# Kernel tuning notes

Measured on AMD Instinct MI355X. Metric: run time of the kernel, lower is better.

The kernel has to match this reference:

```python
import jax, jax.numpy as jnp
import numpy as np

EPS = 1e-6
NUM_SPECIAL = 4
NUM_HEADS = 16


def _rms_norm(x, w, eps=EPS):
    # x: [..., d], normalize over last dim
    var = jnp.mean(jnp.square(x), axis=-1, keepdims=True)
    return x * jax.lax.rsqrt(var + eps) * w


def _rotate_half(x):
    d = x.shape[-1] // 2
    return jnp.concatenate([-x[..., d:], x[..., :d]], axis=-1)


def _apply_rotary(q, k, cos, sin):
    # q,k: [B,H,N,hd]; cos,sin: [N,hd] -> broadcast [1,1,N,hd]
    cos = cos[None, None, :, :]
    sin = sin[None, None, :, :]
    q_out = q * cos + _rotate_half(q) * sin
    k_out = k * cos + _rotate_half(k) * sin
    return q_out, k_out


def _make_2d_mask(seq_len, num_special, window):
    # special tokens attend / are attended fully; patches use 2D local box
    patch_len = seq_len - num_special
    gs = int(round(patch_len ** 0.5))
    idx = jnp.arange(seq_len)
    special = idx < num_special
    p = idx - num_special
    row = p // gs
    col = p % gs
    special_case = special[:, None] | special[None, :]
    swa = (jnp.abs(row[:, None] - row[None, :]) <= window) & (
        jnp.abs(col[:, None] - col[None, :]) <= window)
    return special_case | swa  # [N, N] bool


def setup_inputs() -> dict:
    key = jax.random.key(0)
    ks = jax.random.split(key, 7)
    B, N, C = 4, 1028, 1024
    hd = C // NUM_HEADS
    return {
        "hidden_states": jax.random.normal(ks[0], (B, N, C), dtype=jnp.float32),
        "cos": jax.random.uniform(ks[1], (N, hd), dtype=jnp.float32),
        "sin": jax.random.uniform(ks[2], (N, hd), dtype=jnp.float32),
        "qkv_w": jax.random.normal(ks[3], (3 * C, C), dtype=jnp.float32) * (C ** -0.5),
        "out_w": jax.random.normal(ks[4], (C, C), dtype=jnp.float32) * (C ** -0.5),
        "norm_q_w": jnp.ones((hd,), dtype=jnp.float32),
        "norm_k_w": jnp.ones((hd,), dtype=jnp.float32),
        "sliding_window": 2,
    }


def reference(hidden_states, cos, sin, qkv_w, out_w, norm_q_w, norm_k_w, sliding_window):
    B, N, C = hidden_states.shape
    H = NUM_HEADS
    hd = C // H

    # fused QKV projection (nn.Linear: x @ W^T)
    qkv = jnp.einsum('bnc,dc->bnd', hidden_states, qkv_w)
    qkv = qkv.reshape(B, N, 3, H, hd).transpose(2, 0, 3, 1, 4)  # [3,B,H,N,hd]
    q, k, v = qkv[0], qkv[1], qkv[2]

    # per-head-dim RMSNorm on q and k
    q = _rms_norm(q, norm_q_w)
    k = _rms_norm(k, norm_k_w)

    # RoPE
    q, k = _apply_rotary(q, k, cos, sin)

    # 2D sliding-window + special-token mask
    mask = _make_2d_mask(N, NUM_SPECIAL, sliding_window)  # [N,N]

    scale = 1.0 / jnp.sqrt(jnp.asarray(hd, dtype=q.dtype))
    scores = jnp.einsum('bhqd,bhkd->bhqk', q, k) * scale
    neg = jnp.asarray(jnp.finfo(scores.dtype).min, dtype=scores.dtype)
    scores = jnp.where(mask[None, None, :, :], scores, neg)
    probs = jax.nn.softmax(scores, axis=-1)
    attn = jnp.einsum('bhqk,bhkd->bhqd', probs, v)  # [B,H,N,hd]

    attn = attn.transpose(0, 2, 1, 3).reshape(B, N, C)
    return jnp.einsum('bnc,dc->bnd', attn, out_w)
```

## Files before the change

kernel.cpp:

```cpp
#include <hip/hip_runtime.h>
#include <hip/hip_bf16.h>
#include <stdint.h>

typedef __bf16 bf16;
typedef __attribute__((ext_vector_type(8))) __bf16 bf16x8;
typedef __attribute__((ext_vector_type(4))) __bf16 bf16x4;
typedef __attribute__((ext_vector_type(4))) float f32x4;

#define NSEQ 1028
#define CDIM 1024
#define NHEADS 16
#define HD 64
#define BHN 64
#define NPAD 1088
#define M_REAL 4112
#define MTILES 33

static __device__ __forceinline__ void async_copy16(bf16* lds, const bf16* g) {
  __builtin_amdgcn_global_load_lds(
      (const __attribute__((address_space(1))) uint32_t*)g,
      (__attribute__((address_space(3))) uint32_t*)lds, 16, 0, 0);
}

__global__ __launch_bounds__(256) void cast3_kernel(
    const float* __restrict__ s0, bf16* __restrict__ d0, long n0,
    const float* __restrict__ s1, bf16* __restrict__ d1, long n1,
    const float* __restrict__ s2, bf16* __restrict__ d2, long n2) {
  long total = n0 + n1 + n2;
  long t = (long)blockIdx.x * 256 + threadIdx.x;
  long stride = (long)gridDim.x * 256;
  for (long j = t * 4; j < total; j += stride * 4) {
    const float* s; bf16* d; long jj = j;
    if (jj < n0) { s = s0; d = d0; }
    else if (jj < n0 + n1) { s = s1; d = d1; jj -= n0; }
    else { s = s2; d = d2; jj -= n0 + n1; }
    float4 v = *(const float4*)(s + jj);
    bf16x4 o;
    o[0] = (bf16)v.x; o[1] = (bf16)v.y; o[2] = (bf16)v.z; o[3] = (bf16)v.w;
    *(bf16x4*)(d + jj) = o;
  }
}

template <int EPI, int NSTRIP, int BN, int DEPTH>
__global__ __launch_bounds__(256, 4) void gemm_bf16_kernel(
    const bf16* __restrict__ A, const bf16* __restrict__ Bm,
    bf16* __restrict__ q_bf, bf16* __restrict__ k_bf, bf16* __restrict__ v_raw,
    float* __restrict__ outF,
    const float* __restrict__ cosb, const float* __restrict__ sinb,
    const float* __restrict__ nqw, const float* __restrict__ nkw) {
  constexpr int K = CDIM;
  constexpr int N = NSTRIP * 8 * BN;
  constexpr int HN = BN / 2;
  constexpr int NJ = HN / 16;
  constexpr int BSLOTS = (BN * 4) / 256;
  constexpr int LPS = 2 + BSLOTS;
  constexpr int NBUF = DEPTH + 1;
  __shared__ __attribute__((aligned(16))) bf16 As[NBUF][128 * 32];
  __shared__ __attribute__((aligned(16))) bf16 Bs[NBUF][BN * 32];
  const int tid = threadIdx.x;
  const int lane = tid & 63;
  const int wid = tid >> 6;
  const int wr = wid >> 1, wc = wid & 1;
  const int l15 = lane & 15, l4 = lane >> 4;

  const int xcd = blockIdx.x & 7;
  const int pos = blockIdx.x >> 3;
  const int nloc = pos % NSTRIP;
  const int mi = pos / NSTRIP;
  const int n0 = (xcd * NSTRIP + nloc) * BN;
  const int m0 = (mi < MTILES - 1) ? (mi << 7) : (M_REAL - 128);

  f32x4 acc[4][NJ] = {};

  size_t a_base[2], b_base[BSLOTS];
#pragma unroll
  for (int s = 0; s < 2; s++) {
    int c = tid + s * 256;
    int u = c ^ ((c >> 3) & 7);
    a_base[s] = (size_t)(m0 + (u >> 2)) * K + ((u & 3) << 3);
  }
#pragma unroll
  for (int s = 0; s < BSLOTS; s++) {
    int c = tid + s * 256;
    int u = c ^ ((c >> 3) & 7);
    b_base[s] = (size_t)(n0 + (u >> 2)) * K + ((u & 3) << 3);
  }

#define STAGE(bufi, ktof)                                                   \
  {                                                                         \
    _Pragma("unroll")                                                       \
    for (int s = 0; s < 2; s++)                                             \
      async_copy16(&As[bufi][(tid + s * 256) * 8], A + a_base[s] + (ktof)); \
    _Pragma("unroll")                                                       \
    for (int s = 0; s < BSLOTS; s++)                                        \
      async_copy16(&Bs[bufi][(tid + s * 256) * 8], Bm + b_base[s] + (ktof));\
  }

  const int nt = K >> 5;
#pragma unroll
  for (int d = 0; d < DEPTH; d++) STAGE(d, d << 5);

  for (int t = 0; t < nt; ++t) {
    if (t + DEPTH < nt) STAGE((t + DEPTH) % NBUF, (t + DEPTH) << 5);
    const int left = nt - 1 - t;
    if (left >= DEPTH) {
      asm volatile("s_waitcnt vmcnt(%0)" :: "i"(DEPTH * LPS) : "memory");
    } else if (left == 1) {
      asm volatile("s_waitcnt vmcnt(%0)" :: "i"(LPS) : "memory");
    } else {
      asm volatile("s_waitcnt vmcnt(0)" ::: "memory");
    }
    __builtin_amdgcn_s_barrier();

    const int cur = t % NBUF;
    bf16x8 af[4], bfr[NJ];
#pragma unroll
    for (int i = 0; i < 4; i++) {
      int u = ((wr * 64 + i * 16 + l15) << 2) | l4;
      af[i] = *(const bf16x8*)&As[cur][(u ^ ((u >> 3) & 7)) << 3];
    }
#pragma unroll
    for (int j = 0; j < NJ; j++) {
      int u = ((wc * HN + j * 16 + l15) << 2) | l4;
      bfr[j] = *(const bf16x8*)&Bs[cur][(u ^ ((u >> 3) & 7)) << 3];
    }

#pragma unroll
    for (int i = 0; i < 4; i++)
#pragma unroll
      for (int j = 0; j < NJ; j++)
        acc[i][j] = __builtin_amdgcn_mfma_f32_16x16x32_bf16(af[i], bfr[j], acc[i][j], 0, 0, 0);

    asm volatile("s_waitcnt lgkmcnt(0)" ::: "memory");
    __builtin_amdgcn_s_barrier();
  }
#undef STAGE

  if (EPI == 0) {
    const int d_base = n0 + wc * 64;
    const int tsel = d_base >> 10;
    const int hh = (d_base & 1023) >> 6;
    if (tsel == 2) {
#pragma unroll
      for (int i = 0; i < 4; i++)
#pragma unroll
        for (int r = 0; r < 4; r++) {
          int m = m0 + wr * 64 + i * 16 + l4 * 4 + r;
          int b = m / NSEQ, n = m % NSEQ;
          size_t rb = ((size_t)(b * NHEADS + hh) * NSEQ + n) * HD;
#pragma unroll
          for (int j = 0; j < NJ; j++)
            v_raw[rb + j * 16 + l15] = (bf16)acc[i][j][r];
        }
    } else {
      const float* wn = (tsel == 0) ? nqw : nkw;
      bf16* dst = (tsel == 0) ? q_bf : k_bf;
      float wv[NJ];
#pragma unroll
      for (int j = 0; j < NJ; j++) wv[j] = wn[j * 16 + l15];
#pragma unroll
      for (int i = 0; i < 4; i++)
#pragma unroll
        for (int r = 0; r < 4; r++) {
          int m = m0 + wr * 64 + i * 16 + l4 * 4 + r;
          float ss = 0.0f;
#pragma unroll
          for (int j = 0; j < NJ; j++) { float x = acc[i][j][r]; ss += x * x; }
          ss += __shfl_xor(ss, 1);
          ss += __shfl_xor(ss, 2);
          ss += __shfl_xor(ss, 4);
          ss += __shfl_xor(ss, 8);
          float rms = rsqrtf(ss * (1.0f / HD) + 1e-6f);
          int b = m / NSEQ, n = m % NSEQ;
          float qn[NJ];
#pragma unroll
          for (int j = 0; j < NJ; j++) qn[j] = acc[i][j][r] * rms * wv[j];
          size_t rb = ((size_t)(b * NHEADS + hh) * NPAD + n) * HD;
#pragma unroll
          for (int j = 0; j < NJ; j++) {
            float c = cosb[n * HD + j * 16 + l15];
            float s = sinb[n * HD + j * 16 + l15];
            float rot = (j < 2) ? -qn[j + 2] : qn[j - 2];
            dst[rb + j * 16 + l15] = (bf16)(qn[j] * c + rot * s);
          }
        }
    }
  } else {
#pragma unroll
    for (int i = 0; i < 4; i++)
#pragma unroll
      for (int j = 0; j < NJ; j++) {
        int d = n0 + wc * HN + j * 16 + l15;
        int mrow = m0 + wr * 64 + i * 16 + l4 * 4;
#pragma unroll
        for (int r = 0; r < 4; r++) {
          int m = mrow + r;
          outF[(size_t)m * N + d] = acc[i][j][r];
        }
      }
  }
}

__global__ __launch_bounds__(256) void v_transpose_kernel(const bf16* __restrict__ v_raw,
                                                          bf16* __restrict__ vT) {
  __shared__ bf16 tile[64][65];
  int bh = blockIdx.y, c = blockIdx.x;
  int tid = threadIdx.x;
#pragma unroll
  for (int jj = 0; jj < 16; jj++) {
    int idx = tid + jj * 256;
    int i = idx >> 6, e = idx & 63;
    int n = (c == 0) ? i : (64 * c - 60 + i);
    bool ok = (c == 0) ? (i < 4) : (n < NSEQ);
    tile[i][e] = ok ? v_raw[((size_t)bh * NSEQ + n) * HD + e] : (bf16)0.0f;
  }
  __syncthreads();
#pragma unroll
  for (int jj = 0; jj < 16; jj++) {
    int idx = tid + jj * 256;
    int e = idx >> 6, i = idx & 63;
    vT[((size_t)bh * HD + e) * NPAD + 64 * c + i] = tile[i][e];
  }
}

__global__ __launch_bounds__(256) void attn_kernel(
    const bf16* __restrict__ Q, const bf16* __restrict__ Kb, const bf16* __restrict__ Vt,
    bf16* __restrict__ att, const int* __restrict__ winp) {
  __shared__ __attribute__((aligned(16))) bf16 P_s[4][16][72];
  __shared__ __attribute__((aligned(16))) bf16 KV[2][2][64 * 64];
  const int bh = blockIdx.y, qt = blockIdx.x;
  const int W = winp[0];
  const int tid = threadIdx.x, w = tid >> 6, lane = tid & 63;
  const int l15 = lane & 15, l4 = lane >> 4;
  const size_t qkbase = (size_t)bh * NPAD * HD;
  const size_t vtb = (size_t)bh * HD * NPAD;
  const bool is_spec = (qt == 16);
  const int b = bh >> 4, h = bh & 15;

  const int qrow0 = is_spec ? 0 : (4 + qt * 64 + w * 16);
  bf16x8 aq0 = *(const bf16x8*)&Q[qkbase + (size_t)(qrow0 + l15) * HD + l4 * 8];
  bf16x8 aq1 = *(const bf16x8*)&Q[qkbase + (size_t)(qrow0 + l15) * HD + 32 + l4 * 8];

  float mrow[4], lrow[4];
  f32x4 o[4] = {};
#pragma unroll
  for (int r = 0; r < 4; r++) { mrow[r] = -1e30f; lrow[r] = 0.0f; }

  if (!is_spec) {
    int ta = ((2 * qt - W + 64) >> 1) - 32;
    int tb = (2 * qt + 1 + W) >> 1;
    ta = ta < 0 ? 0 : ta;
    tb = tb > 15 ? 15 : tb;
    const int P = tb - ta + 2;

    int srow[2], sch[2];
#pragma unroll
    for (int s = 0; s < 2; s++) {
      int c = tid + s * 256;
      int u = c ^ ((c >> 3) & 7);
      srow[s] = u >> 3; sch[s] = u & 7;
    }

#define STAGE_KV(bufi, p)                                                     \
    {                                                                         \
      int kr = (p) == 0 ? 0 : 4 + (ta + (p) - 1) * 64;                        \
      int vc = (p) == 0 ? 0 : 64 + (ta + (p) - 1) * 64;                       \
      _Pragma("unroll")                                                       \
      for (int s = 0; s < 2; s++)                                             \
        async_copy16(&KV[bufi][0][(tid + s * 256) * 8],                       \
                     Kb + qkbase + (size_t)(kr + srow[s]) * HD + sch[s] * 8); \
      _Pragma("unroll")                                                       \
      for (int s = 0; s < 2; s++)                                             \
        async_copy16(&KV[bufi][1][(tid + s * 256) * 8],                       \
                     Vt + vtb + (size_t)srow[s] * NPAD + vc + sch[s] * 8);    \
    }

    STAGE_KV(0, 0);

    for (int p = 0; p < P; ++p) {
      if (p + 1 < P) {
        STAGE_KV((p + 1) & 1, p + 1);
        asm volatile("s_waitcnt vmcnt(4)" ::: "memory");
      } else {
        asm volatile("s_waitcnt vmcnt(0)" ::: "memory");
      }
      __builtin_amdgcn_s_barrier();

      const int cur = p & 1;
      const bool sp = (p == 0);
      const int tau = ta + p - 1;

      f32x4 sacc[4] = {};
#pragma unroll
      for (int kf = 0; kf < 4; kf++) {
        int u0 = ((kf * 16 + l15) << 3) | l4;
        int u1 = ((kf * 16 + l15) << 3) | (4 + l4);
        bf16x8 b0 = *(const bf16x8*)&KV[cur][0][(u0 ^ ((u0 >> 3) & 7)) << 3];
        bf16x8 b1 = *(const bf16x8*)&KV[cur][0][(u1 ^ ((u1 >> 3) & 7)) << 3];
        sacc[kf] = __builtin_amdgcn_mfma_f32_16x16x32_bf16(aq0, b0, sacc[kf], 0, 0, 0);
        sacc[kf] = __builtin_amdgcn_mfma_f32_16x16x32_bf16(aq1, b1, sacc[kf], 0, 0, 0);
      }

      float pvv[4][4];
#pragma unroll
      for (int kf = 0; kf < 4; kf++)
#pragma unroll
        for (int r = 0; r < 4; r++) {
          float s = sacc[kf][r] * 0.125f;
          bool valid;
          if (sp) {
            valid = (kf == 0) && (l15 < 4);
          } else {
            int p_k = tau * 64 + kf * 16 + l15;
            int p_q = qt * 64 + w * 16 + l4 * 4 + r;
            int dr = (p_q >> 5) - (p_k >> 5); dr = dr < 0 ? -dr : dr;
            int dc = (p_q & 31) - (p_k & 31); dc = dc < 0 ? -dc : dc;
            valid = (dr <= W) && (dc <= W);
          }
          pvv[kf][r] = valid ? s : -1e30f;
        }

#pragma unroll
      for (int r = 0; r < 4; r++) {
        float mx = fmaxf(fmaxf(pvv[0][r], pvv[1][r]), fmaxf(pvv[2][r], pvv[3][r]));
#pragma unroll
        for (int mm = 1; mm < 16; mm <<= 1) mx = fmaxf(mx, __shfl_xor(mx, mm));
        float mnew = fmaxf(mrow[r], mx);
        float scale = __expf(mrow[r] - mnew);
        float rs = 0.0f;
#pragma unroll
        for (int kf = 0; kf < 4; kf++) {
          float pp = __expf(pvv[kf][r] - mnew);
          pvv[kf][r] = pp;
          rs += pp;
        }
#pragma unroll
        for (int mm = 1; mm < 16; mm <<= 1) rs += __shfl_xor(rs, mm);
        lrow[r] = lrow[r] * scale + rs;
        mrow[r] = mnew;
#pragma unroll
        for (int f = 0; f < 4; f++) o[f][r] *= scale;
      }

#pragma unroll
      for (int kf = 0; kf < 4; kf++)
#pragma unroll
        for (int r = 0; r < 4; r++)
          P_s[w][l4 * 4 + r][kf * 16 + l15] = (bf16)pvv[kf][r];

      bf16x8 pa0 = *(const bf16x8*)&P_s[w][l15][l4 * 8];
      bf16x8 pa1 = *(const bf16x8*)&P_s[w][l15][32 + l4 * 8];
#pragma unroll
      for (int f = 0; f < 4; f++) {
        int u0 = ((f * 16 + l15) << 3) | l4;
        int u1 = ((f * 16 + l15) << 3) | (4 + l4);
        bf16x8 v0 = *(const bf16x8*)&KV[cur][1][(u0 ^ ((u0 >> 3) & 7)) << 3];
        bf16x8 v1 = *(const bf16x8*)&KV[cur][1][(u1 ^ ((u1 >> 3) & 7)) << 3];
        o[f] = __builtin_amdgcn_mfma_f32_16x16x32_bf16(pa0, v0, o[f], 0, 0, 0);
        o[f] = __builtin_amdgcn_mfma_f32_16x16x32_bf16(pa1, v1, o[f], 0, 0, 0);
      }

      asm volatile("s_waitcnt lgkmcnt(0)" ::: "memory");
      __builtin_amdgcn_s_barrier();
    }
#undef STAGE_KV

#pragma unroll
    for (int f = 0; f < 4; f++)
#pragma unroll
      for (int r = 0; r < 4; r++) {
        int n = qrow0 + l4 * 4 + r;
        att[((size_t)(b * NSEQ + n)) * CDIM + h * HD + f * 16 + l15] =
            (bf16)(o[f][r] / lrow[r]);
      }
  } else {
    float* o_sf = (float*)&KV[0][0][0];
    float* ml_sf = o_sf + 4 * 4 * 64;

    for (int p = w; p <= 16; p += 4) {
      const bool sp = (p == 0);
      const int tau = p - 1;
      const int krow0 = sp ? 0 : (4 + tau * 64);
      const int vcol0 = sp ? 0 : (64 + tau * 64);

      f32x4 sacc[4] = {};
#pragma unroll
      for (int kf = 0; kf < 4; kf++) {
        const bf16* kp = &Kb[qkbase + (size_t)(krow0 + kf * 16 + l15) * HD];
        bf16x8 b0 = *(const bf16x8*)(kp + l4 * 8);
        bf16x8 b1 = *(const bf16x8*)(kp + 32 + l4 * 8);
        sacc[kf] = __builtin_amdgcn_mfma_f32_16x16x32_bf16(aq0, b0, sacc[kf], 0, 0, 0);
        sacc[kf] = __builtin_amdgcn_mfma_f32_16x16x32_bf16(aq1, b1, sacc[kf], 0, 0, 0);
      }

      float pvv[4][4];
#pragma unroll
      for (int kf = 0; kf < 4; kf++)
#pragma unroll
        for (int r = 0; r < 4; r++) {
          float s = sacc[kf][r] * 0.125f;
          bool valid = sp ? ((kf == 0) && (l15 < 4)) : true;
          pvv[kf][r] = valid ? s : -1e30f;
        }

#pragma unroll
      for (int r = 0; r < 4; r++) {
        float mx = fmaxf(fmaxf(pvv[0][r], pvv[1][r]), fmaxf(pvv[2][r], pvv[3][r]));
#pragma unroll
        for (int mm = 1; mm < 16; mm <<= 1) mx = fmaxf(mx, __shfl_xor(mx, mm));
        float mnew = fmaxf(mrow[r], mx);
        float scale = __expf(mrow[r] - mnew);
        float rs = 0.0f;
#pragma unroll
        for (int kf = 0; kf < 4; kf++) {
          float pp = __expf(pvv[kf][r] - mnew);
          pvv[kf][r] = pp;
          rs += pp;
        }
#pragma unroll
        for (int mm = 1; mm < 16; mm <<= 1) rs += __shfl_xor(rs, mm);
        lrow[r] = lrow[r] * scale + rs;
        mrow[r] = mnew;
#pragma unroll
        for (int f = 0; f < 4; f++) o[f][r] *= scale;
      }

#pragma unroll
      for (int kf = 0; kf < 4; kf++)
#pragma unroll
        for (int r = 0; r < 4; r++)
          P_s[w][l4 * 4 + r][kf * 16 + l15] = (bf16)pvv[kf][r];

      bf16x8 pa0 = *(const bf16x8*)&P_s[w][l15][l4 * 8];
      bf16x8 pa1 = *(const bf16x8*)&P_s[w][l15][32 + l4 * 8];
#pragma unroll
      for (int f = 0; f < 4; f++) {
        const bf16* vp = &Vt[vtb + (size_t)(f * 16 + l15) * NPAD + vcol0];
        bf16x8 v0 = *(const bf16x8*)(vp + l4 * 8);
        bf16x8 v1 = *(const bf16x8*)(vp + 32 + l4 * 8);
        o[f] = __builtin_amdgcn_mfma_f32_16x16x32_bf16(pa0, v0, o[f], 0, 0, 0);
        o[f] = __builtin_amdgcn_mfma_f32_16x16x32_bf16(pa1, v1, o[f], 0, 0, 0);
      }
    }

    if (l4 == 0) {
#pragma unroll
      for (int f = 0; f < 4; f++)
#pragma unroll
        for (int r = 0; r < 4; r++) o_sf[(w * 4 + r) * 64 + f * 16 + l15] = o[f][r];
      if (l15 == 0)
#pragma unroll
        for (int r = 0; r < 4; r++) {
          ml_sf[(w * 2 + 0) * 16 + r] = mrow[r];
          ml_sf[(w * 2 + 1) * 16 + r] = lrow[r];
        }
    }
    __syncthreads();
    int row = tid >> 6, dim = tid & 63;
    float M = -1e30f;
#pragma unroll
    for (int ww = 0; ww < 4; ww++) M = fmaxf(M, ml_sf[(ww * 2) * 16 + row]);
    float L = 0.0f, val = 0.0f;
#pragma unroll
    for (int ww = 0; ww < 4; ww++) {
      float e = __expf(ml_sf[(ww * 2) * 16 + row] - M);
      L += e * ml_sf[(ww * 2 + 1) * 16 + row];
      val += e * o_sf[(ww * 4 + row) * 64 + dim];
    }
    att[((size_t)(b * NSEQ + row)) * CDIM + h * HD + dim] = (bf16)(val / L);
  }
}

extern "C" void kernel_launch(void* const* d_in, const int* in_sizes, int n_in,
                              void* d_out, int out_size, void* d_ws, size_t ws_size,
                              hipStream_t stream) {
  const float* hidden = (const float*)d_in[0];
  const float* cosb = (const float*)d_in[1];
  const float* sinb = (const float*)d_in[2];
  const float* qkv_w = (const float*)d_in[3];
  const float* out_w = (const float*)d_in[4];
  const float* norm_q_w = (const float*)d_in[5];
  const float* norm_k_w = (const float*)d_in[6];
  const int* win = (const int*)d_in[7];
  float* out = (float*)d_out;

  char* ws = (char*)d_ws;
  size_t off = 0;
  auto alloc = [&](size_t bytes) {
    char* p = ws + off;
    off += (bytes + 255) & ~(size_t)255;
    return p;
  };
  bf16* A_bf  = (bf16*)alloc((size_t)M_REAL * CDIM * 2);
  bf16* W1    = (bf16*)alloc((size_t)3 * CDIM * CDIM * 2);
  bf16* W2    = (bf16*)alloc((size_t)CDIM * CDIM * 2);
  bf16* v_raw = (bf16*)alloc((size_t)BHN * NSEQ * HD * 2);
  bf16* q_bf  = (bf16*)alloc((size_t)BHN * NPAD * HD * 2);
  bf16* k_bf  = (bf16*)alloc((size_t)BHN * NPAD * HD * 2);
  bf16* vT    = (bf16*)alloc((size_t)BHN * HD * NPAD * 2);
  bf16* att   = (bf16*)alloc((size_t)M_REAL * CDIM * 2);
  (void)ws_size; (void)in_sizes; (void)n_in; (void)out_size;

  cast3_kernel<<<2048, 256, 0, stream>>>(
      hidden, A_bf, (long)M_REAL * CDIM,
      qkv_w, W1, (long)3 * CDIM * CDIM,
      out_w, W2, (long)CDIM * CDIM);

  gemm_bf16_kernel<0, 3, 128, 1><<<792, 256, 0, stream>>>(
      A_bf, W1, q_bf, k_bf, v_raw, nullptr, cosb, sinb, norm_q_w, norm_k_w);
  v_transpose_kernel<<<dim3(17, 64), 256, 0, stream>>>(v_raw, vT);
  attn_kernel<<<dim3(17, 64), 256, 0, stream>>>(q_bf, k_bf, vT, att, win);
  gemm_bf16_kernel<1, 2, 64, 1><<<528, 256, 0, stream>>>(
      att, W2, nullptr, nullptr, nullptr, out, nullptr, nullptr, nullptr, nullptr);
}
```

Measured before the change: 110.0 us.

## Process 128 query rows per attention block to reuse staged K/V tiles

Each attention workgroup now covers 128 patch query rows, with each wave handling two 16-row fragments, instead of 64 rows. The grid drops from 17 to 9 blocks per head. Each K/V tile staged into LDS is therefore reused by twice as many queries, cutting global K/V traffic and staging overhead. In exchange there are fewer blocks (576) for the GPU's compute units, more registers per wave, and a slightly wider key-tile range per block.

```diff
diff --git a/kernel.cpp b/kernel.cpp
--- a/kernel.cpp
+++ b/kernel.cpp
@@ -234,21 +234,27 @@
   const int l15 = lane & 15, l4 = lane >> 4;
   const size_t qkbase = (size_t)bh * NPAD * HD;
   const size_t vtb = (size_t)bh * HD * NPAD;
-  const bool is_spec = (qt == 16);
+  const bool is_spec = (qt == 8);
   const int b = bh >> 4, h = bh & 15;
 
-  const int qrow0 = is_spec ? 0 : (4 + qt * 64 + w * 16);
-  bf16x8 aq0 = *(const bf16x8*)&Q[qkbase + (size_t)(qrow0 + l15) * HD + l4 * 8];
-  bf16x8 aq1 = *(const bf16x8*)&Q[qkbase + (size_t)(qrow0 + l15) * HD + 32 + l4 * 8];
-
-  float mrow[4], lrow[4];
-  f32x4 o[4] = {};
-#pragma unroll
-  for (int r = 0; r < 4; r++) { mrow[r] = -1e30f; lrow[r] = 0.0f; }
-
   if (!is_spec) {
-    int ta = ((2 * qt - W + 64) >> 1) - 32;
-    int tb = (2 * qt + 1 + W) >> 1;
+    const int qrow0 = 4 + qt * 128 + w * 32;
+    bf16x8 aq[2][2];
+#pragma unroll
+    for (int f = 0; f < 2; f++) {
+      aq[f][0] = *(const bf16x8*)&Q[qkbase + (size_t)(qrow0 + f * 16 + l15) * HD + l4 * 8];
+      aq[f][1] = *(const bf16x8*)&Q[qkbase + (size_t)(qrow0 + f * 16 + l15) * HD + 32 + l4 * 8];
+    }
+
+    float mrow[2][4], lrow[2][4];
+    f32x4 o[2][4] = {};
+#pragma unroll
+    for (int f = 0; f < 2; f++)
+#pragma unroll
+      for (int r = 0; r < 4; r++) { mrow[f][r] = -1e30f; lrow[f][r] = 0.0f; }
+
+    int ta = ((4 * qt - W + 64) >> 1) - 32;
+    int tb = (4 * qt + 3 + W) >> 1;
     ta = ta < 0 ? 0 : ta;
     tb = tb > 15 ? 15 : tb;
     const int P = tb - ta + 2;
@@ -290,74 +296,77 @@
       const bool sp = (p == 0);
       const int tau = ta + p - 1;
 
-      f32x4 sacc[4] = {};
-#pragma unroll
-      for (int kf = 0; kf < 4; kf++) {
-        int u0 = ((kf * 16 + l15) << 3) | l4;
-        int u1 = ((kf * 16 + l15) << 3) | (4 + l4);
-        bf16x8 b0 = *(const bf16x8*)&KV[cur][0][(u0 ^ ((u0 >> 3) & 7)) << 3];
-        bf16x8 b1 = *(const bf16x8*)&KV[cur][0][(u1 ^ ((u1 >> 3) & 7)) << 3];
-        sacc[kf] = __builtin_amdgcn_mfma_f32_16x16x32_bf16(aq0, b0, sacc[kf], 0, 0, 0);
-        sacc[kf] = __builtin_amdgcn_mfma_f32_16x16x32_bf16(aq1, b1, sacc[kf], 0, 0, 0);
-      }
-
-      float pvv[4][4];
-#pragma unroll
-      for (int kf = 0; kf < 4; kf++)
-#pragma unroll
-        for (int r = 0; r < 4; r++) {
-          float s = sacc[kf][r] * 0.125f;
-          bool valid;
-          if (sp) {
-            valid = (kf == 0) && (l15 < 4);
-          } else {
-            int p_k = tau * 64 + kf * 16 + l15;
-            int p_q = qt * 64 + w * 16 + l4 * 4 + r;
-            int dr = (p_q >> 5) - (p_k >> 5); dr = dr < 0 ? -dr : dr;
-            int dc = (p_q & 31) - (p_k & 31); dc = dc < 0 ? -dc : dc;
-            valid = (dr <= W) && (dc <= W);
+#pragma unroll
+      for (int f = 0; f < 2; f++) {
+        f32x4 sacc[4] = {};
+#pragma unroll
+        for (int kf = 0; kf < 4; kf++) {
+          int u0 = ((kf * 16 + l15) << 3) | l4;
+          int u1 = ((kf * 16 + l15) << 3) | (4 + l4);
+          bf16x8 b0 = *(const bf16x8*)&KV[cur][0][(u0 ^ ((u0 >> 3) & 7)) << 3];
+          bf16x8 b1 = *(const bf16x8*)&KV[cur][0][(u1 ^ ((u1 >> 3) & 7)) << 3];
+          sacc[kf] = __builtin_amdgcn_mfma_f32_16x16x32_bf16(aq[f][0], b0, sacc[kf], 0, 0, 0);
+          sacc[kf] = __builtin_amdgcn_mfma_f32_16x16x32_bf16(aq[f][1], b1, sacc[kf], 0, 0, 0);
+        }
+
+        float pvv[4][4];
+#pragma unroll
+        for (int kf = 0; kf < 4; kf++)
+#pragma unroll
+          for (int r = 0; r < 4; r++) {
+            float s = sacc[kf][r] * 0.125f;
+            bool valid;
+            if (sp) {
+              valid = (kf == 0) && (l15 < 4);
+            } else {
+              int p_k = tau * 64 + kf * 16 + l15;
+              int p_q = qt * 128 + w * 32 + f * 16 + l4 * 4 + r;
+              int dr = (p_q >> 5) - (p_k >> 5); dr = dr < 0 ? -dr : dr;
+              int dc = (p_q & 31) - (p_k & 31); dc = dc < 0 ? -dc : dc;
+              valid = (dr <= W) && (dc <= W);
+            }
+            pvv[kf][r] = valid ? s : -1e30f;
           }
-          pvv[kf][r] = valid ? s : -1e30f;
-        }
-
-#pragma unroll
-      for (int r = 0; r < 4; r++) {
-        float mx = fmaxf(fmaxf(pvv[0][r], pvv[1][r]), fmaxf(pvv[2][r], pvv[3][r]));
-#pragma unroll
-        for (int mm = 1; mm < 16; mm <<= 1) mx = fmaxf(mx, __shfl_xor(mx, mm));
-        float mnew = fmaxf(mrow[r], mx);
-        float scale = __expf(mrow[r] - mnew);
-        float rs = 0.0f;
-#pragma unroll
-        for (int kf = 0; kf < 4; kf++) {
-          float pp = __expf(pvv[kf][r] - mnew);
-          pvv[kf][r] = pp;
-          rs += pp;
-        }
-#pragma unroll
-        for (int mm = 1; mm < 16; mm <<= 1) rs += __shfl_xor(rs, mm);
-        lrow[r] = lrow[r] * scale + rs;
-        mrow[r] = mnew;
-#pragma unroll
-        for (int f = 0; f < 4; f++) o[f][r] *= scale;
-      }
-
-#pragma unroll
-      for (int kf = 0; kf < 4; kf++)
-#pragma unroll
-        for (int r = 0; r < 4; r++)
-          P_s[w][l4 * 4 + r][kf * 16 + l15] = (bf16)pvv[kf][r];
-
-      bf16x8 pa0 = *(const bf16x8*)&P_s[w][l15][l4 * 8];
-      bf16x8 pa1 = *(const bf16x8*)&P_s[w][l15][32 + l4 * 8];
-#pragma unroll
-      for (int f = 0; f < 4; f++) {
-        int u0 = ((f * 16 + l15) << 3) | l4;
-        int u1 = ((f * 16 + l15) << 3) | (4 + l4);
-        bf16x8 v0 = *(const bf16x8*)&KV[cur][1][(u0 ^ ((u0 >> 3) & 7)) << 3];
-        bf16x8 v1 = *(const bf16x8*)&KV[cur][1][(u1 ^ ((u1 >> 3) & 7)) << 3];
-        o[f] = __builtin_amdgcn_mfma_f32_16x16x32_bf16(pa0, v0, o[f], 0, 0, 0);
-        o[f] = __builtin_amdgcn_mfma_f32_16x16x32_bf16(pa1, v1, o[f], 0, 0, 0);
+
+#pragma unroll
+        for (int r = 0; r < 4; r++) {
+          float mx = fmaxf(fmaxf(pvv[0][r], pvv[1][r]), fmaxf(pvv[2][r], pvv[3][r]));
+#pragma unroll
+          for (int mm = 1; mm < 16; mm <<= 1) mx = fmaxf(mx, __shfl_xor(mx, mm));
+          float mnew = fmaxf(mrow[f][r], mx);
+          float scale = __expf(mrow[f][r] - mnew);
+          float rs = 0.0f;
+#pragma unroll
+          for (int kf = 0; kf < 4; kf++) {
+            float pp = __expf(pvv[kf][r] - mnew);
+            pvv[kf][r] = pp;
+            rs += pp;
+          }
+#pragma unroll
+          for (int mm = 1; mm < 16; mm <<= 1) rs += __shfl_xor(rs, mm);
+          lrow[f][r] = lrow[f][r] * scale + rs;
+          mrow[f][r] = mnew;
+#pragma unroll
+          for (int ff = 0; ff < 4; ff++) o[f][ff][r] *= scale;
+        }
+
+#pragma unroll
+        for (int kf = 0; kf < 4; kf++)
+#pragma unroll
+          for (int r = 0; r < 4; r++)
+            P_s[w][l4 * 4 + r][kf * 16 + l15] = (bf16)pvv[kf][r];
+
+        bf16x8 pa0 = *(const bf16x8*)&P_s[w][l15][l4 * 8];
+        bf16x8 pa1 = *(const bf16x8*)&P_s[w][l15][32 + l4 * 8];
+#pragma unroll
+        for (int ff = 0; ff < 4; ff++) {
+          int u0 = ((ff * 16 + l15) << 3) | l4;
+          int u1 = ((ff * 16 + l15) << 3) | (4 + l4);
+          bf16x8 v0 = *(const bf16x8*)&KV[cur][1][(u0 ^ ((u0 >> 3) & 7)) << 3];
+          bf16x8 v1 = *(const bf16x8*)&KV[cur][1][(u1 ^ ((u1 >> 3) & 7)) << 3];
+          o[f][ff] = __builtin_amdgcn_mfma_f32_16x16x32_bf16(pa0, v0, o[f][ff], 0, 0, 0);
+          o[f][ff] = __builtin_amdgcn_mfma_f32_16x16x32_bf16(pa1, v1, o[f][ff], 0, 0, 0);
+        }
       }
 
       asm volatile("s_waitcnt lgkmcnt(0)" ::: "memory");
@@ -366,14 +375,23 @@
 #undef STAGE_KV
 
 #pragma unroll
-    for (int f = 0; f < 4; f++)
-#pragma unroll
-      for (int r = 0; r < 4; r++) {
-        int n = qrow0 + l4 * 4 + r;
-        att[((size_t)(b * NSEQ + n)) * CDIM + h * HD + f * 16 + l15] =
-            (bf16)(o[f][r] / lrow[r]);
-      }
+    for (int f = 0; f < 2; f++)
+#pragma unroll
+      for (int ff = 0; ff < 4; ff++)
+#pragma unroll
+        for (int r = 0; r < 4; r++) {
+          int n = qrow0 + f * 16 + l4 * 4 + r;
+          att[((size_t)(b * NSEQ + n)) * CDIM + h * HD + ff * 16 + l15] =
+              (bf16)(o[f][ff][r] / lrow[f][r]);
+        }
   } else {
+    bf16x8 aq0 = *(const bf16x8*)&Q[qkbase + (size_t)l15 * HD + l4 * 8];
+    bf16x8 aq1 = *(const bf16x8*)&Q[qkbase + (size_t)l15 * HD + 32 + l4 * 8];
+    float mrow[4], lrow[4];
+    f32x4 o[4] = {};
+#pragma unroll
+    for (int r = 0; r < 4; r++) { mrow[r] = -1e30f; lrow[r] = 0.0f; }
+
     float* o_sf = (float*)&KV[0][0][0];
     float* ml_sf = o_sf + 4 * 4 * 64;
 
@@ -509,7 +527,7 @@
   gemm_bf16_kernel<0, 3, 128, 1><<<792, 256, 0, stream>>>(
       A_bf, W1, q_bf, k_bf, v_raw, nullptr, cosb, sinb, norm_q_w, norm_k_w);
   v_transpose_kernel<<<dim3(17, 64), 256, 0, stream>>>(v_raw, vT);
-  attn_kernel<<<dim3(17, 64), 256, 0, stream>>>(q_bf, k_bf, vT, att, win);
+  attn_kernel<<<dim3(9, 64), 256, 0, stream>>>(q_bf, k_bf, vT, att, win);
   gemm_bf16_kernel<1, 2, 64, 1><<<528, 256, 0, stream>>>(
       att, W2, nullptr, nullptr, nullptr, out, nullptr, nullptr, nullptr, nullptr);
 }
```

New measurement: 120.6 us. +9.7%, slower.
